# Kernel tuning notes

Measured on AMD Instinct MI355X. Metric: run time of the kernel, lower is better.

Reference implementation:

```python
import jax, jax.numpy as jnp
import numpy as np

N_NODES = 50000
N_GRAPHS = 128
IN_DIM = 512
HID = 512
N_LAYERS = 3


def setup_inputs() -> dict:
    key = jax.random.key(0)
    ks = jax.random.split(key, 12)
    inp = {
        "x": jax.random.normal(ks[0], (N_NODES, IN_DIM), dtype=jnp.float32),
        "walk2": jax.random.randint(ks[1], (3, N_NODES), 0, N_NODES, dtype=jnp.int32),
        "walk3": jax.random.randint(ks[2], (4, N_NODES), 0, N_NODES, dtype=jnp.int32),
        "walk4": jax.random.randint(ks[3], (5, N_NODES), 0, N_NODES, dtype=jnp.int32),
        "batch": jnp.sort(jax.random.randint(ks[4], (N_NODES,), 0, N_GRAPHS, dtype=jnp.int32)),
    }
    dims = [IN_DIM, HID, HID]
    for i in range(N_LAYERS):
        scale = 1.0 / np.sqrt(dims[i])
        inp[f"W{i}"] = jax.random.normal(ks[5 + i], (dims[i], HID), dtype=jnp.float32) * scale
        inp[f"b{i}"] = jnp.zeros((HID,), dtype=jnp.float32)
    return inp


def _gather_sum(z, walk):
    # walk: [L, N] node indices -> sum of gathered embeddings, [N, H]
    L, N = walk.shape
    return jnp.take(z, walk.reshape(-1), axis=0).reshape(L, N, z.shape[1]).sum(0)


def reference(x, walk2, walk3, walk4, batch, W0, b0, W1, b1, W2, b2):
    layers = [(W0, b0), (W1, b1), (W2, b2)]
    path_batch = jnp.take(batch, walk2[0])  # [N]
    counts = jax.ops.segment_sum(jnp.ones((path_batch.shape[0],), jnp.float32),
                                 path_batch, num_segments=N_GRAPHS)
    denom = jnp.maximum(counts, 1.0)[:, None]  # avoid div-by-zero for empty graphs
    z = x
    g = []
    for W, b in layers:
        z = z @ W + b  # [N, H]
        path_emb = _gather_sum(z, walk2) + _gather_sum(z, walk3) + _gather_sum(z, walk4)
        pooled = jax.ops.segment_sum(path_emb, path_batch, num_segments=N_GRAPHS) / denom
        g.append(pooled)
    return jnp.concatenate(g, axis=1)  # [N_GRAPHS, 3*H]
```

## Files before the change

kernel.cpp:

```cpp
#include <hip/hip_runtime.h>

#define N_NODES 50000
#define N_GRAPHS 128
#define HID 512

#define KSPAN  512
#define KSPLIT 98
#define KPAD   (KSPAN * KSPLIT)
#define NPANEL (KPAD / 16)

#define C8_OFF     0
#define C8_BYTES   ((size_t)N_GRAPHS * KPAD)
#define PSUM_OFF   (C8_OFF + C8_BYTES)
#define PSUM_BYTES ((size_t)N_GRAPHS * HID * 4)
#define COUNTS_OFF (PSUM_OFF + PSUM_BYTES)
#define ZERO_BYTES (COUNTS_OFF + 512)
#define APACK_OFF  ZERO_BYTES
#define APACK_BYTES ((size_t)NPANEL * 4 * 64 * 16)
#define PART_OFF   (APACK_OFF + APACK_BYTES)
#define PART_BYTES ((size_t)KSPLIT * N_GRAPHS * HID * 4)

typedef __attribute__((ext_vector_type(8))) short bf16x8;
typedef __attribute__((ext_vector_type(16))) float f32x16;
typedef const __attribute__((address_space(1))) void* gas_t;
typedef __attribute__((address_space(3))) void* las_t;

__global__ __launch_bounds__(256)
void build_c_kernel(const int* __restrict__ w2, const int* __restrict__ w3,
                    const int* __restrict__ w4, const int* __restrict__ batch,
                    unsigned int* __restrict__ C32, int* __restrict__ counts) {
    __shared__ int hist[N_GRAPHS];
    const int t = threadIdx.x;
    if (t < N_GRAPHS) hist[t] = 0;
    __syncthreads();
    const int i = blockIdx.x * 256 + t;
    if (i < N_NODES) {
        const int a = w2[i];
        const int g = batch[a];
        atomicAdd(&hist[g], 1);
        unsigned int* row = C32 + (size_t)g * (KPAD / 4);
        int nn[12];
        nn[0]  = a;
        nn[1]  = w2[N_NODES + i];
        nn[2]  = w2[2 * N_NODES + i];
        nn[3]  = w3[i];
        nn[4]  = w3[N_NODES + i];
        nn[5]  = w3[2 * N_NODES + i];
        nn[6]  = w3[3 * N_NODES + i];
        nn[7]  = w4[i];
        nn[8]  = w4[N_NODES + i];
        nn[9]  = w4[2 * N_NODES + i];
        nn[10] = w4[3 * N_NODES + i];
        nn[11] = w4[4 * N_NODES + i];
#pragma unroll
        for (int j = 0; j < 12; ++j) {
            const int nd = nn[j];
            atomicAdd(&row[nd >> 2], 1u << ((nd & 3) * 8));
        }
    }
    __syncthreads();
    if (t < N_GRAPHS) { const int hv = hist[t]; if (hv) atomicAdd(&counts[t], hv); }
}

__device__ inline unsigned pack_bf16(unsigned a, unsigned b) {
    return (__builtin_bit_cast(unsigned, (float)a) >> 16) |
           (__builtin_bit_cast(unsigned, (float)b) & 0xFFFF0000u);
}

__global__ __launch_bounds__(256)
void c8_to_apack_kernel(const unsigned char* __restrict__ C8,
                        uint4* __restrict__ Apack) {
    const int kp = blockIdx.x;
    const int t = threadIdx.x;
    const int mt = t >> 6;
    const int l = t & 63;
    const int row = mt * 32 + (l & 31);
    const int k0 = kp * 16 + 8 * (l >> 5);
    const uint2 b = *(const uint2*)(C8 + (size_t)row * KPAD + k0);
    uint4 o;
    o.x = pack_bf16(b.x & 0xFFu, (b.x >> 8) & 0xFFu);
    o.y = pack_bf16((b.x >> 16) & 0xFFu, b.x >> 24);
    o.z = pack_bf16(b.y & 0xFFu, (b.y >> 8) & 0xFFu);
    o.w = pack_bf16((b.y >> 16) & 0xFFu, b.y >> 24);
    Apack[(size_t)(kp * 4 + mt) * 64 + l] = o;
}

template <int ATOMIC>
__global__ __launch_bounds__(512, 4)
void pool_gemm4_kernel(const float* __restrict__ x,
                       const uint4* __restrict__ Apack,
                       float* __restrict__ dst) {
    __shared__ float lbuf[128 * 128];
    const int t = threadIdx.x;
    const int lane = t & 63;
    const int w = t >> 6;
    const int n = lane & 31;
    const int h = lane >> 5;
    const int nt = w & 3;
    const int mh = w >> 2;
    const int colbase = blockIdx.x * 128;
    const int ks = blockIdx.y;
    const int kbase = ks * KSPAN;

    f32x16 acc0, acc1;
#pragma unroll
    for (int r = 0; r < 16; ++r) { acc0[r] = 0.f; acc1[r] = 0.f; }

    for (int ch = 0; ch < 4; ++ch) {
        const int k0 = kbase + ch * 128;
        if (k0 >= N_NODES) break;
        if (k0 + 128 <= N_NODES) {
#pragma unroll
            for (int i = 0; i < 8; ++i) {
                const int rbase = w * 16 + 2 * i;
                const float* gp = x + (size_t)(k0 + rbase + (lane >> 5)) * HID
                                    + colbase + (lane & 31) * 4;
                las_t lp = (las_t)&lbuf[rbase * 128];
                __builtin_amdgcn_global_load_lds((gas_t)gp, lp, 16, 0, 0);
            }
        } else {
#pragma unroll
            for (int j = 0; j < 32; ++j) {
                const int idx = t + j * 512;
                const int r = idx >> 7, c = idx & 127;
                const int kg = k0 + r;
                lbuf[idx] = (kg < N_NODES) ? x[(size_t)kg * HID + colbase + c] : 0.f;
            }
        }
        __syncthreads();

        const int kp0 = k0 >> 4;
#pragma unroll
        for (int s = 0; s < 8; ++s) {
            unsigned bw[4];
#pragma unroll
            for (int j2 = 0; j2 < 4; ++j2) {
                const int kl = s * 16 + 8 * h + 2 * j2;
                const unsigned u0 = __builtin_bit_cast(unsigned, lbuf[kl * 128 + nt * 32 + n]);
                const unsigned u1 = __builtin_bit_cast(unsigned, lbuf[(kl + 1) * 128 + nt * 32 + n]);
                bw[j2] = (u0 >> 16) | (u1 & 0xFFFF0000u);
            }
            const uint4 bu = make_uint4(bw[0], bw[1], bw[2], bw[3]);
            const bf16x8 bf = __builtin_bit_cast(bf16x8, bu);
            const bf16x8 a0 = __builtin_bit_cast(bf16x8,
                Apack[(size_t)((kp0 + s) * 4 + 2 * mh) * 64 + lane]);
            const bf16x8 a1 = __builtin_bit_cast(bf16x8,
                Apack[(size_t)((kp0 + s) * 4 + 2 * mh + 1) * 64 + lane]);
            acc0 = __builtin_amdgcn_mfma_f32_32x32x16_bf16(a0, bf, acc0, 0, 0, 0);
            acc1 = __builtin_amdgcn_mfma_f32_32x32x16_bf16(a1, bf, acc1, 0, 0, 0);
        }
        __syncthreads();
    }

    float* outp = ATOMIC ? dst : dst + (size_t)ks * (N_GRAPHS * HID);
    const int col = colbase + nt * 32 + n;
#pragma unroll
    for (int r = 0; r < 16; ++r) {
        const int row0 = mh * 64 + (r & 3) + 8 * (r >> 2) + 4 * h;
        if (ATOMIC) {
            atomicAdd(&outp[(size_t)row0 * HID + col], acc0[r]);
            atomicAdd(&outp[(size_t)(row0 + 32) * HID + col], acc1[r]);
        } else {
            outp[(size_t)row0 * HID + col] = acc0[r];
            outp[(size_t)(row0 + 32) * HID + col] = acc1[r];
        }
    }
}

__global__ __launch_bounds__(256)
void reduce_part_kernel(const float* __restrict__ part, float* __restrict__ Psum) {
    const int id = blockIdx.x * 256 + threadIdx.x;
    float s0 = 0.f, s1 = 0.f;
    for (int k = 0; k + 2 <= KSPLIT; k += 2) {
        s0 += part[(size_t)k * (N_GRAPHS * HID) + id];
        s1 += part[(size_t)(k + 1) * (N_GRAPHS * HID) + id];
    }
    Psum[id] = s0 + s1;
}

__global__ __launch_bounds__(256)
void layer_gemm_kernel(const float* __restrict__ A, int lda, int scaleA,
                       const float* __restrict__ W,
                       const float* __restrict__ bias,
                       const int* __restrict__ counts,
                       float* __restrict__ out) {
    __shared__ float Alds[16][128];
    const int ct = blockIdx.x, rt = blockIdx.y, ksb = blockIdx.z;
    const int t = threadIdx.x;
    const int cc = ct * 64 + (t & 63);
    const int wv = t >> 6;
    const int k0 = ksb * 128;

    for (int idx = t; idx < 16 * 32; idx += 256) {
        const int rr = idx >> 5;
        const int kk = (idx & 31) * 4;
        const int row = rt * 16 + rr;
        float4 v = *(const float4*)&A[(size_t)row * lda + k0 + kk];
        if (scaleA) {
            const float inv = 1.f / (float)max(counts[row], 1);
            v.x *= inv; v.y *= inv; v.z *= inv; v.w *= inv;
        }
        *(float4*)&Alds[rr][kk] = v;
    }
    __syncthreads();

    const int r0 = rt * 16 + wv * 4;
    float a0 = 0.f, a1 = 0.f, a2 = 0.f, a3 = 0.f;
#pragma unroll 8
    for (int k = 0; k < 128; ++k) {
        const float wval = W[(size_t)(k0 + k) * HID + cc];
        a0 += Alds[wv * 4 + 0][k] * wval;
        a1 += Alds[wv * 4 + 1][k] * wval;
        a2 += Alds[wv * 4 + 2][k] * wval;
        a3 += Alds[wv * 4 + 3][k] * wval;
    }
    if (ksb == 0) {
        const float bc = bias[cc];
        a0 += (counts[r0 + 0] > 0 ? 12.f : 0.f) * bc;
        a1 += (counts[r0 + 1] > 0 ? 12.f : 0.f) * bc;
        a2 += (counts[r0 + 2] > 0 ? 12.f : 0.f) * bc;
        a3 += (counts[r0 + 3] > 0 ? 12.f : 0.f) * bc;
    }
    atomicAdd(&out[(size_t)(r0 + 0) * 1536 + cc], a0);
    atomicAdd(&out[(size_t)(r0 + 1) * 1536 + cc], a1);
    atomicAdd(&out[(size_t)(r0 + 2) * 1536 + cc], a2);
    atomicAdd(&out[(size_t)(r0 + 3) * 1536 + cc], a3);
}

extern "C" void kernel_launch(void* const* d_in, const int* in_sizes, int n_in,
                              void* d_out, int out_size, void* d_ws, size_t ws_size,
                              hipStream_t stream) {
    const float* x     = (const float*)d_in[0];
    const int*   w2    = (const int*)d_in[1];
    const int*   w3    = (const int*)d_in[2];
    const int*   w4    = (const int*)d_in[3];
    const int*   batch = (const int*)d_in[4];
    const float* W0    = (const float*)d_in[5];
    const float* b0    = (const float*)d_in[6];
    const float* W1    = (const float*)d_in[7];
    const float* b1    = (const float*)d_in[8];
    const float* W2    = (const float*)d_in[9];
    const float* b2    = (const float*)d_in[10];
    float* out = (float*)d_out;

    unsigned char* ws  = (unsigned char*)d_ws;
    unsigned int* C32  = (unsigned int*)(ws + C8_OFF);
    float* Psum        = (float*)(ws + PSUM_OFF);
    int* counts        = (int*)(ws + COUNTS_OFF);
    uint4* Apack       = (uint4*)(ws + APACK_OFF);
    float* part        = (float*)(ws + PART_OFF);
    const bool use_part = ws_size >= PART_OFF + PART_BYTES;

    hipMemsetAsync(d_ws, 0, ZERO_BYTES, stream);
    hipMemsetAsync(d_out, 0, (size_t)out_size * 4, stream);

    build_c_kernel<<<(N_NODES + 255) / 256, 256, 0, stream>>>(w2, w3, w4, batch, C32, counts);
    c8_to_apack_kernel<<<NPANEL, 256, 0, stream>>>((const unsigned char*)C32, Apack);

    if (use_part) {
        pool_gemm4_kernel<0><<<dim3(4, KSPLIT), 512, 0, stream>>>(x, Apack, part);
        reduce_part_kernel<<<256, 256, 0, stream>>>(part, Psum);
    } else {
        pool_gemm4_kernel<1><<<dim3(4, KSPLIT), 512, 0, stream>>>(x, Apack, Psum);
    }

    layer_gemm_kernel<<<dim3(8, 8, 4), 256, 0, stream>>>(Psum, HID, 1, W0, b0, counts, out);
    layer_gemm_kernel<<<dim3(8, 8, 4), 256, 0, stream>>>(out, 1536, 0, W1, b1, counts, out + 512);
    layer_gemm_kernel<<<dim3(8, 8, 4), 256, 0, stream>>>(out + 512, 1536, 0, W2, b2, counts, out + 1024);
}
```

Measured before the change: 276.4 us.

## Replace LDS-staged pooling GEMM with register-pipelined per-wave K-split and LDS reduction

The pooling GEMM (C x X) no longer stages X tiles through LDS with global_load_lds. Each wave now loads its B operand straight from global memory into registers, using a 3-deep software pipeline over 18 K-steps, and packs to bf16 with a perm instruction. Each wave owns its own K-slice of a 64x64 output region. The four waves in a block are summed through LDS before writing, which cuts the number of partial buffers from 98 to 44 and so reduces the later reduce pass. The risk is uncoalesced strided scalar loads from x and higher register pressure.

After: 266.8 us. -3.5%, faster.

```diff
diff --git a/kernel.cpp b/kernel.cpp
--- a/kernel.cpp
+++ b/kernel.cpp
@@ -4,10 +4,12 @@
 #define N_GRAPHS 128
 #define HID 512
 
-#define KSPAN  512
-#define KSPLIT 98
-#define KPAD   (KSPAN * KSPLIT)
-#define NPANEL (KPAD / 16)
+#define KSPAN   288
+#define NSTEP   18
+#define KS2     44
+#define KSPLIT  (KS2 * 4)
+#define KPAD    (KSPAN * KSPLIT)
+#define NPANEL  (KPAD / 16)
 
 #define C8_OFF     0
 #define C8_BYTES   ((size_t)N_GRAPHS * KPAD)
@@ -18,12 +20,10 @@
 #define APACK_OFF  ZERO_BYTES
 #define APACK_BYTES ((size_t)NPANEL * 4 * 64 * 16)
 #define PART_OFF   (APACK_OFF + APACK_BYTES)
-#define PART_BYTES ((size_t)KSPLIT * N_GRAPHS * HID * 4)
+#define PART_BYTES ((size_t)KS2 * N_GRAPHS * HID * 4)
 
 typedef __attribute__((ext_vector_type(8))) short bf16x8;
 typedef __attribute__((ext_vector_type(16))) float f32x16;
-typedef const __attribute__((address_space(1))) void* gas_t;
-typedef __attribute__((address_space(3))) void* las_t;
 
 __global__ __launch_bounds__(256)
 void build_c_kernel(const int* __restrict__ w2, const int* __restrict__ w3,
@@ -85,84 +85,128 @@
     Apack[(size_t)(kp * 4 + mt) * 64 + l] = o;
 }
 
+template <int GUARD>
+__device__ inline void issue_b(const float* __restrict__ xp, int krow,
+                               unsigned (&u)[16]) {
+#pragma unroll
+    for (int j = 0; j < 8; ++j) {
+        int k = krow + j;
+        if (GUARD) k = min(k, N_NODES - 1);
+        const float* p = xp + (size_t)k * HID;
+        u[j]     = __builtin_bit_cast(unsigned, p[0]);
+        u[8 + j] = __builtin_bit_cast(unsigned, p[32]);
+    }
+}
+
+__device__ inline f32x16 mfma_bf16(bf16x8 a, bf16x8 b, f32x16 c) {
+    return __builtin_amdgcn_mfma_f32_32x32x16_bf16(a, b, c, 0, 0, 0);
+}
+
+__device__ inline unsigned bpack(unsigned u0, unsigned u1) {
+    return __builtin_amdgcn_perm(u1, u0, 0x07060302u);
+}
+
+__device__ inline void step_mfma(const unsigned (&u)[16], const uint4 (&a)[2],
+                                 f32x16 (&acc)[2][2]) {
+    unsigned d0[4], d1[4];
+#pragma unroll
+    for (int jj = 0; jj < 4; ++jj) {
+        d0[jj] = bpack(u[2 * jj], u[2 * jj + 1]);
+        d1[jj] = bpack(u[8 + 2 * jj], u[8 + 2 * jj + 1]);
+    }
+    const bf16x8 b0 = __builtin_bit_cast(bf16x8, make_uint4(d0[0], d0[1], d0[2], d0[3]));
+    const bf16x8 b1 = __builtin_bit_cast(bf16x8, make_uint4(d1[0], d1[1], d1[2], d1[3]));
+    const bf16x8 a0 = __builtin_bit_cast(bf16x8, a[0]);
+    const bf16x8 a1 = __builtin_bit_cast(bf16x8, a[1]);
+    acc[0][0] = mfma_bf16(a0, b0, acc[0][0]);
+    acc[0][1] = mfma_bf16(a0, b1, acc[0][1]);
+    acc[1][0] = mfma_bf16(a1, b0, acc[1][0]);
+    acc[1][1] = mfma_bf16(a1, b1, acc[1][1]);
+}
+
+template <int GUARD>
+__device__ inline void run_k(const float* __restrict__ xp,
+                             const uint4* __restrict__ Apack,
+                             int kbase, int h, int lane, int rm,
+                             f32x16 (&acc)[2][2]) {
+    unsigned bu[3][16];
+    uint4 au[3][2];
+    const int kp0 = kbase >> 4;
+#pragma unroll
+    for (int s = 0; s < 3; ++s) {
+        issue_b<GUARD>(xp, kbase + s * 16 + 8 * h, bu[s]);
+        au[s][0] = Apack[(size_t)((kp0 + s) * 4 + rm * 2) * 64 + lane];
+        au[s][1] = Apack[(size_t)((kp0 + s) * 4 + rm * 2 + 1) * 64 + lane];
+    }
+#pragma unroll
+    for (int s = 0; s < NSTEP; ++s) {
+        const int slot = s % 3;
+        step_mfma(bu[slot], au[slot], acc);
+        if (s + 3 < NSTEP) {
+            issue_b<GUARD>(xp, kbase + (s + 3) * 16 + 8 * h, bu[slot]);
+            au[slot][0] = Apack[(size_t)((kp0 + s + 3) * 4 + rm * 2) * 64 + lane];
+            au[slot][1] = Apack[(size_t)((kp0 + s + 3) * 4 + rm * 2 + 1) * 64 + lane];
+        }
+    }
+}
+
 template <int ATOMIC>
-__global__ __launch_bounds__(512, 4)
-void pool_gemm4_kernel(const float* __restrict__ x,
+__global__ __launch_bounds__(256, 3)
+void pool_gemm5_kernel(const float* __restrict__ x,
                        const uint4* __restrict__ Apack,
                        float* __restrict__ dst) {
-    __shared__ float lbuf[128 * 128];
+    __shared__ float red[3][2][64 * 16];
     const int t = threadIdx.x;
     const int lane = t & 63;
     const int w = t >> 6;
     const int n = lane & 31;
     const int h = lane >> 5;
-    const int nt = w & 3;
-    const int mh = w >> 2;
-    const int colbase = blockIdx.x * 128;
-    const int ks = blockIdx.y;
+    const int region = blockIdx.x;
+    const int rm = region & 1;
+    const int rn = region >> 1;
+    const int ks = blockIdx.y * 4 + w;
     const int kbase = ks * KSPAN;
 
-    f32x16 acc0, acc1;
-#pragma unroll
-    for (int r = 0; r < 16; ++r) { acc0[r] = 0.f; acc1[r] = 0.f; }
-
-    for (int ch = 0; ch < 4; ++ch) {
-        const int k0 = kbase + ch * 128;
-        if (k0 >= N_NODES) break;
-        if (k0 + 128 <= N_NODES) {
-#pragma unroll
-            for (int i = 0; i < 8; ++i) {
-                const int rbase = w * 16 + 2 * i;
-                const float* gp = x + (size_t)(k0 + rbase + (lane >> 5)) * HID
-                                    + colbase + (lane & 31) * 4;
-                las_t lp = (las_t)&lbuf[rbase * 128];
-                __builtin_amdgcn_global_load_lds((gas_t)gp, lp, 16, 0, 0);
-            }
-        } else {
-#pragma unroll
-            for (int j = 0; j < 32; ++j) {
-                const int idx = t + j * 512;
-                const int r = idx >> 7, c = idx & 127;
-                const int kg = k0 + r;
-                lbuf[idx] = (kg < N_NODES) ? x[(size_t)kg * HID + colbase + c] : 0.f;
-            }
-        }
+    f32x16 acc[2][2];
+#pragma unroll
+    for (int p = 0; p < 2; ++p)
+#pragma unroll
+        for (int q = 0; q < 2; ++q)
+#pragma unroll
+            for (int r = 0; r < 16; ++r) acc[p][q][r] = 0.f;
+
+    const float* xp = x + rn * 64 + n;
+
+    if (kbase + KSPAN <= N_NODES) {
+        run_k<0>(xp, Apack, kbase, h, lane, rm, acc);
+    } else if (kbase < N_NODES) {
+        run_k<1>(xp, Apack, kbase, h, lane, rm, acc);
+    }
+
+    float* outp = ATOMIC ? dst : dst + (size_t)blockIdx.y * (N_GRAPHS * HID);
+#pragma unroll
+    for (int p = 0; p < 2; ++p) {
         __syncthreads();
-
-        const int kp0 = k0 >> 4;
-#pragma unroll
-        for (int s = 0; s < 8; ++s) {
-            unsigned bw[4];
-#pragma unroll
-            for (int j2 = 0; j2 < 4; ++j2) {
-                const int kl = s * 16 + 8 * h + 2 * j2;
-                const unsigned u0 = __builtin_bit_cast(unsigned, lbuf[kl * 128 + nt * 32 + n]);
-                const unsigned u1 = __builtin_bit_cast(unsigned, lbuf[(kl + 1) * 128 + nt * 32 + n]);
-                bw[j2] = (u0 >> 16) | (u1 & 0xFFFF0000u);
-            }
-            const uint4 bu = make_uint4(bw[0], bw[1], bw[2], bw[3]);
-            const bf16x8 bf = __builtin_bit_cast(bf16x8, bu);
-            const bf16x8 a0 = __builtin_bit_cast(bf16x8,
-                Apack[(size_t)((kp0 + s) * 4 + 2 * mh) * 64 + lane]);
-            const bf16x8 a1 = __builtin_bit_cast(bf16x8,
-                Apack[(size_t)((kp0 + s) * 4 + 2 * mh + 1) * 64 + lane]);
-            acc0 = __builtin_amdgcn_mfma_f32_32x32x16_bf16(a0, bf, acc0, 0, 0, 0);
-            acc1 = __builtin_amdgcn_mfma_f32_32x32x16_bf16(a1, bf, acc1, 0, 0, 0);
+        if (w > 0) {
+#pragma unroll
+            for (int q = 0; q < 2; ++q)
+#pragma unroll
+                for (int i = 0; i < 16; ++i)
+                    red[w - 1][q][i * 64 + lane] = acc[p][q][i];
         }
         __syncthreads();
-    }
-
-    float* outp = ATOMIC ? dst : dst + (size_t)ks * (N_GRAPHS * HID);
-    const int col = colbase + nt * 32 + n;
-#pragma unroll
-    for (int r = 0; r < 16; ++r) {
-        const int row0 = mh * 64 + (r & 3) + 8 * (r >> 2) + 4 * h;
-        if (ATOMIC) {
-            atomicAdd(&outp[(size_t)row0 * HID + col], acc0[r]);
-            atomicAdd(&outp[(size_t)(row0 + 32) * HID + col], acc1[r]);
-        } else {
-            outp[(size_t)row0 * HID + col] = acc0[r];
-            outp[(size_t)(row0 + 32) * HID + col] = acc1[r];
+        if (w == 0) {
+#pragma unroll
+            for (int q = 0; q < 2; ++q)
+#pragma unroll
+                for (int i = 0; i < 16; ++i) {
+                    const float v = acc[p][q][i] + red[0][q][i * 64 + lane] +
+                                    red[1][q][i * 64 + lane] + red[2][q][i * 64 + lane];
+                    const int row = rm * 64 + p * 32 + (i & 3) + 8 * (i >> 2) + 4 * h;
+                    const int col = rn * 64 + q * 32 + n;
+                    if (ATOMIC) atomicAdd(&outp[(size_t)row * HID + col], v);
+                    else        outp[(size_t)row * HID + col] = v;
+                }
         }
     }
 }
@@ -171,7 +215,7 @@
 void reduce_part_kernel(const float* __restrict__ part, float* __restrict__ Psum) {
     const int id = blockIdx.x * 256 + threadIdx.x;
     float s0 = 0.f, s1 = 0.f;
-    for (int k = 0; k + 2 <= KSPLIT; k += 2) {
+    for (int k = 0; k + 2 <= KS2; k += 2) {
         s0 += part[(size_t)k * (N_GRAPHS * HID) + id];
         s1 += part[(size_t)(k + 1) * (N_GRAPHS * HID) + id];
     }
@@ -258,10 +302,10 @@
     c8_to_apack_kernel<<<NPANEL, 256, 0, stream>>>((const unsigned char*)C32, Apack);
 
     if (use_part) {
-        pool_gemm4_kernel<0><<<dim3(4, KSPLIT), 512, 0, stream>>>(x, Apack, part);
+        pool_gemm5_kernel<0><<<dim3(16, KS2), 256, 0, stream>>>(x, Apack, part);
         reduce_part_kernel<<<256, 256, 0, stream>>>(part, Psum);
     } else {
-        pool_gemm4_kernel<1><<<dim3(4, KSPLIT), 512, 0, stream>>>(x, Apack, Psum);
+        pool_gemm5_kernel<1><<<dim3(16, KS2), 256, 0, stream>>>(x, Apack, Psum);
     }
 
     layer_gemm_kernel<<<dim3(8, 8, 4), 256, 0, stream>>>(Psum, HID, 1, W0, b0, counts, out);
```

## Restructure pooling GEMM to per-wave column slabs with full-M tiles and finer K split

Applied to the files above, without the earlier changes.

Replaces the pooling GEMM so that each block covers all 512 columns and all 128 graph rows for a 208-node K span, launching 241 blocks instead of a 4x98 grid. Each wave owns a private 64-column LDS slab, which removes block-wide __syncthreads. It loads the A panels for all four M tiles into registers and issues 8 MFMAs per K step, so each packed B fragment is reused across four A tiles. bf16 packing now uses v_perm. The trade-off is a much larger partial buffer (241 slices) for the reduce kernel to read, and higher register pressure (launch bounds 2 blocks per CU).

After: 291.0 us. +5.3%, slower.

```diff
diff --git a/kernel.cpp b/kernel.cpp
--- a/kernel.cpp
+++ b/kernel.cpp
@@ -4,10 +4,10 @@
 #define N_GRAPHS 128
 #define HID 512
 
-#define KSPAN  512
-#define KSPLIT 98
-#define KPAD   (KSPAN * KSPLIT)
-#define NPANEL (KPAD / 16)
+#define KSPAN   208
+#define KSPLIT  241
+#define KPAD    (KSPAN * KSPLIT)
+#define NPANEL  (KPAD / 16)
 
 #define C8_OFF     0
 #define C8_BYTES   ((size_t)N_GRAPHS * KPAD)
@@ -85,96 +85,128 @@
     Apack[(size_t)(kp * 4 + mt) * 64 + l] = o;
 }
 
+__device__ inline unsigned bpack(unsigned u0, unsigned u1) {
+    return __builtin_amdgcn_perm(u1, u0, 0x07060302u);
+}
+
+__device__ inline f32x16 mfma_bf16(bf16x8 a, bf16x8 b, f32x16 c) {
+    return __builtin_amdgcn_mfma_f32_32x32x16_bf16(a, b, c, 0, 0, 0);
+}
+
+template <int ROWS>
+__device__ inline void do_chunk(const float* __restrict__ x,
+                                const uint4* __restrict__ Apack,
+                                float* __restrict__ lb,
+                                int w, int lane, int s0, int kp0,
+                                f32x16 (&acc)[4][2]) {
+    const int cg = w * 64 + (lane & 15) * 4;
+    const int rsub = lane >> 4;
+
+    if (s0 + ROWS <= N_NODES) {
+#pragma unroll
+        for (int i = 0; i < ROWS / 4; ++i) {
+            const float* gp = x + (size_t)(s0 + 4 * i + rsub) * HID + cg;
+            las_t lp = (las_t)(lb + 4 * i * 64);
+            __builtin_amdgcn_global_load_lds((gas_t)gp, lp, 16, 0, 0);
+        }
+    } else {
+#pragma unroll
+        for (int i = 0; i < ROWS / 4; ++i) {
+            const int row = min(s0 + 4 * i + rsub, N_NODES - 1);
+            const float4 v = *(const float4*)(x + (size_t)row * HID + cg);
+            *(float4*)(lb + (4 * i + rsub) * 64 + (lane & 15) * 4) = v;
+        }
+    }
+
+    uint4 a[ROWS / 16][4];
+#pragma unroll
+    for (int s2 = 0; s2 < ROWS / 16; ++s2)
+#pragma unroll
+        for (int mt = 0; mt < 4; ++mt)
+            a[s2][mt] = Apack[(size_t)((kp0 + s2) * 4 + mt) * 64 + lane];
+
+    __builtin_amdgcn_s_waitcnt(0);
+
+    const int n = lane & 31;
+    const int h = lane >> 5;
+#pragma unroll
+    for (int s2 = 0; s2 < ROWS / 16; ++s2) {
+        unsigned b0w[4], b1w[4];
+#pragma unroll
+        for (int jj = 0; jj < 4; ++jj) {
+            const int r0 = s2 * 16 + 8 * h + 2 * jj;
+            const unsigned u00 = __builtin_bit_cast(unsigned, lb[r0 * 64 + n]);
+            const unsigned u01 = __builtin_bit_cast(unsigned, lb[(r0 + 1) * 64 + n]);
+            const unsigned u10 = __builtin_bit_cast(unsigned, lb[r0 * 64 + 32 + n]);
+            const unsigned u11 = __builtin_bit_cast(unsigned, lb[(r0 + 1) * 64 + 32 + n]);
+            b0w[jj] = bpack(u00, u01);
+            b1w[jj] = bpack(u10, u11);
+        }
+        const bf16x8 B0 = __builtin_bit_cast(bf16x8, make_uint4(b0w[0], b0w[1], b0w[2], b0w[3]));
+        const bf16x8 B1 = __builtin_bit_cast(bf16x8, make_uint4(b1w[0], b1w[1], b1w[2], b1w[3]));
+#pragma unroll
+        for (int mt = 0; mt < 4; ++mt) {
+            const bf16x8 af = __builtin_bit_cast(bf16x8, a[s2][mt]);
+            acc[mt][0] = mfma_bf16(af, B0, acc[mt][0]);
+            acc[mt][1] = mfma_bf16(af, B1, acc[mt][1]);
+        }
+    }
+}
+
 template <int ATOMIC>
-__global__ __launch_bounds__(512, 4)
-void pool_gemm4_kernel(const float* __restrict__ x,
+__global__ __launch_bounds__(512, 2)
+void pool_gemm6_kernel(const float* __restrict__ x,
                        const uint4* __restrict__ Apack,
                        float* __restrict__ dst) {
-    __shared__ float lbuf[128 * 128];
+    __shared__ float lbuf[8][32 * 64];
     const int t = threadIdx.x;
     const int lane = t & 63;
     const int w = t >> 6;
+    float* lb = &lbuf[w][0];
+
+    const int kbase = blockIdx.x * KSPAN;
+    const int kp_base = blockIdx.x * 13;
+
+    f32x16 acc[4][2];
+#pragma unroll
+    for (int mt = 0; mt < 4; ++mt)
+#pragma unroll
+        for (int q = 0; q < 2; ++q)
+#pragma unroll
+            for (int r = 0; r < 16; ++r) acc[mt][q][r] = 0.f;
+
+#pragma unroll
+    for (int ch = 0; ch < 6; ++ch)
+        do_chunk<32>(x, Apack, lb, w, lane, kbase + ch * 32, kp_base + ch * 2, acc);
+    do_chunk<16>(x, Apack, lb, w, lane, kbase + 192, kp_base + 12, acc);
+
     const int n = lane & 31;
     const int h = lane >> 5;
-    const int nt = w & 3;
-    const int mh = w >> 2;
-    const int colbase = blockIdx.x * 128;
-    const int ks = blockIdx.y;
-    const int kbase = ks * KSPAN;
-
-    f32x16 acc0, acc1;
-#pragma unroll
-    for (int r = 0; r < 16; ++r) { acc0[r] = 0.f; acc1[r] = 0.f; }
-
-    for (int ch = 0; ch < 4; ++ch) {
-        const int k0 = kbase + ch * 128;
-        if (k0 >= N_NODES) break;
-        if (k0 + 128 <= N_NODES) {
-#pragma unroll
-            for (int i = 0; i < 8; ++i) {
-                const int rbase = w * 16 + 2 * i;
-                const float* gp = x + (size_t)(k0 + rbase + (lane >> 5)) * HID
-                                    + colbase + (lane & 31) * 4;
-                las_t lp = (las_t)&lbuf[rbase * 128];
-                __builtin_amdgcn_global_load_lds((gas_t)gp, lp, 16, 0, 0);
+    float* outp = ATOMIC ? dst : dst + (size_t)blockIdx.x * (N_GRAPHS * HID);
+#pragma unroll
+    for (int mt = 0; mt < 4; ++mt)
+#pragma unroll
+        for (int q = 0; q < 2; ++q) {
+            const int col = w * 64 + q * 32 + n;
+#pragma unroll
+            for (int i = 0; i < 16; ++i) {
+                const int row = mt * 32 + (i & 3) + 8 * (i >> 2) + 4 * h;
+                if (ATOMIC) atomicAdd(&outp[(size_t)row * HID + col], acc[mt][q][i]);
+                else        outp[(size_t)row * HID + col] = acc[mt][q][i];
             }
-        } else {
-#pragma unroll
-            for (int j = 0; j < 32; ++j) {
-                const int idx = t + j * 512;
-                const int r = idx >> 7, c = idx & 127;
-                const int kg = k0 + r;
-                lbuf[idx] = (kg < N_NODES) ? x[(size_t)kg * HID + colbase + c] : 0.f;
-            }
-        }
-        __syncthreads();
-
-        const int kp0 = k0 >> 4;
-#pragma unroll
-        for (int s = 0; s < 8; ++s) {
-            unsigned bw[4];
-#pragma unroll
-            for (int j2 = 0; j2 < 4; ++j2) {
-                const int kl = s * 16 + 8 * h + 2 * j2;
-                const unsigned u0 = __builtin_bit_cast(unsigned, lbuf[kl * 128 + nt * 32 + n]);
-                const unsigned u1 = __builtin_bit_cast(unsigned, lbuf[(kl + 1) * 128 + nt * 32 + n]);
-                bw[j2] = (u0 >> 16) | (u1 & 0xFFFF0000u);
-            }
-            const uint4 bu = make_uint4(bw[0], bw[1], bw[2], bw[3]);
-            const bf16x8 bf = __builtin_bit_cast(bf16x8, bu);
-            const bf16x8 a0 = __builtin_bit_cast(bf16x8,
-                Apack[(size_t)((kp0 + s) * 4 + 2 * mh) * 64 + lane]);
-            const bf16x8 a1 = __builtin_bit_cast(bf16x8,
-                Apack[(size_t)((kp0 + s) * 4 + 2 * mh + 1) * 64 + lane]);
-            acc0 = __builtin_amdgcn_mfma_f32_32x32x16_bf16(a0, bf, acc0, 0, 0, 0);
-            acc1 = __builtin_amdgcn_mfma_f32_32x32x16_bf16(a1, bf, acc1, 0, 0, 0);
-        }
-        __syncthreads();
-    }
-
-    float* outp = ATOMIC ? dst : dst + (size_t)ks * (N_GRAPHS * HID);
-    const int col = colbase + nt * 32 + n;
-#pragma unroll
-    for (int r = 0; r < 16; ++r) {
-        const int row0 = mh * 64 + (r & 3) + 8 * (r >> 2) + 4 * h;
-        if (ATOMIC) {
-            atomicAdd(&outp[(size_t)row0 * HID + col], acc0[r]);
-            atomicAdd(&outp[(size_t)(row0 + 32) * HID + col], acc1[r]);
-        } else {
-            outp[(size_t)row0 * HID + col] = acc0[r];
-            outp[(size_t)(row0 + 32) * HID + col] = acc1[r];
-        }
-    }
+        }
 }
 
 __global__ __launch_bounds__(256)
 void reduce_part_kernel(const float* __restrict__ part, float* __restrict__ Psum) {
     const int id = blockIdx.x * 256 + threadIdx.x;
     float s0 = 0.f, s1 = 0.f;
-    for (int k = 0; k + 2 <= KSPLIT; k += 2) {
+    int k = 0;
+    for (; k + 2 <= KSPLIT; k += 2) {
         s0 += part[(size_t)k * (N_GRAPHS * HID) + id];
         s1 += part[(size_t)(k + 1) * (N_GRAPHS * HID) + id];
     }
+    for (; k < KSPLIT; ++k) s0 += part[(size_t)k * (N_GRAPHS * HID) + id];
     Psum[id] = s0 + s1;
 }
 
@@ -258,10 +290,10 @@
     c8_to_apack_kernel<<<NPANEL, 256, 0, stream>>>((const unsigned char*)C32, Apack);
 
     if (use_part) {
-        pool_gemm4_kernel<0><<<dim3(4, KSPLIT), 512, 0, stream>>>(x, Apack, part);
+        pool_gemm6_kernel<0><<<KSPLIT, 512, 0, stream>>>(x, Apack, part);
         reduce_part_kernel<<<256, 256, 0, stream>>>(part, Psum);
     } else {
-        pool_gemm4_kernel<1><<<dim3(4, KSPLIT), 512, 0, stream>>>(x, Apack, Psum);
+        pool_gemm6_kernel<1><<<KSPLIT, 512, 0, stream>>>(x, Apack, Psum);
     }
 
     layer_gemm_kernel<<<dim3(8, 8, 4), 256, 0, stream>>>(Psum, HID, 1, W0, b0, counts, out);
```

## Restructure pooled GEMM: stage A in LDS, stream x directly into registers

Applied to the files above, without the earlier changes.

Rewrites the pooling GEMM so each block copies its slice of the packed count matrix into LDS once. Each wave then reads x columns straight from global memory into registers with a two-stage software prefetch and packs them to bf16 with a byte-permute, and each wave computes all 128 graph rows. The K span is halved and the split count doubled, and the grid now uses two column halves instead of four. This drops the LDS staging of x and its barriers, but it issues strided per-row scalar global loads and doubles the partial buffer that the reduction must sum.

Result: slower. 287.8 us (+4.1%).

```diff
diff --git a/kernel.cpp b/kernel.cpp
--- a/kernel.cpp
+++ b/kernel.cpp
@@ -4,10 +4,10 @@
 #define N_GRAPHS 128
 #define HID 512
 
-#define KSPAN  512
-#define KSPLIT 98
-#define KPAD   (KSPAN * KSPLIT)
-#define NPANEL (KPAD / 16)
+#define KSPAN   256
+#define KSPLIT  196
+#define KPAD    (KSPAN * KSPLIT)
+#define NPANEL  (KPAD / 16)
 
 #define C8_OFF     0
 #define C8_BYTES   ((size_t)N_GRAPHS * KPAD)
@@ -22,8 +22,6 @@
 
 typedef __attribute__((ext_vector_type(8))) short bf16x8;
 typedef __attribute__((ext_vector_type(16))) float f32x16;
-typedef const __attribute__((address_space(1))) void* gas_t;
-typedef __attribute__((address_space(3))) void* las_t;
 
 __global__ __launch_bounds__(256)
 void build_c_kernel(const int* __restrict__ w2, const int* __restrict__ w3,
@@ -85,86 +83,98 @@
     Apack[(size_t)(kp * 4 + mt) * 64 + l] = o;
 }
 
+__device__ inline unsigned bpack(unsigned u0, unsigned u1) {
+    return __builtin_amdgcn_perm(u1, u0, 0x07060302u);
+}
+
+__device__ inline f32x16 mfma_bf16(bf16x8 a, bf16x8 b, f32x16 c) {
+    return __builtin_amdgcn_mfma_f32_32x32x16_bf16(a, b, c, 0, 0, 0);
+}
+
+template <int GUARD>
+__device__ inline void issue_b7(const float* __restrict__ xp, int krow,
+                                unsigned (&u)[8]) {
+#pragma unroll
+    for (int j = 0; j < 8; ++j) {
+        int k = krow + j;
+        if (GUARD) k = min(k, N_NODES - 1);
+        u[j] = __builtin_bit_cast(unsigned, xp[(size_t)k * HID]);
+    }
+}
+
+template <int GUARD>
+__device__ inline void run_k7(const float* __restrict__ xp,
+                              const uint4* __restrict__ ldsA,
+                              int kbase, int h, int lane,
+                              f32x16 (&acc)[4]) {
+    unsigned bu[2][8];
+    issue_b7<GUARD>(xp, kbase + 8 * h, bu[0]);
+    issue_b7<GUARD>(xp, kbase + 16 + 8 * h, bu[1]);
+#pragma unroll
+    for (int s = 0; s < KSPAN / 16; ++s) {
+        const int slot = s & 1;
+        uint4 a[4];
+#pragma unroll
+        for (int mt = 0; mt < 4; ++mt)
+            a[mt] = ldsA[(s * 4 + mt) * 64 + lane];
+        unsigned d[4];
+#pragma unroll
+        for (int jj = 0; jj < 4; ++jj)
+            d[jj] = bpack(bu[slot][2 * jj], bu[slot][2 * jj + 1]);
+        const bf16x8 B = __builtin_bit_cast(bf16x8, make_uint4(d[0], d[1], d[2], d[3]));
+        if (s + 2 < KSPAN / 16)
+            issue_b7<GUARD>(xp, kbase + (s + 2) * 16 + 8 * h, bu[slot]);
+#pragma unroll
+        for (int mt = 0; mt < 4; ++mt)
+            acc[mt] = mfma_bf16(__builtin_bit_cast(bf16x8, a[mt]), B, acc[mt]);
+    }
+}
+
 template <int ATOMIC>
 __global__ __launch_bounds__(512, 4)
-void pool_gemm4_kernel(const float* __restrict__ x,
+void pool_gemm7_kernel(const float* __restrict__ x,
                        const uint4* __restrict__ Apack,
                        float* __restrict__ dst) {
-    __shared__ float lbuf[128 * 128];
+    __shared__ uint4 ldsA[(KSPAN / 16) * 4 * 64];
     const int t = threadIdx.x;
     const int lane = t & 63;
     const int w = t >> 6;
     const int n = lane & 31;
     const int h = lane >> 5;
-    const int nt = w & 3;
-    const int mh = w >> 2;
-    const int colbase = blockIdx.x * 128;
+    const int chalf = blockIdx.x;
     const int ks = blockIdx.y;
     const int kbase = ks * KSPAN;
-
-    f32x16 acc0, acc1;
-#pragma unroll
-    for (int r = 0; r < 16; ++r) { acc0[r] = 0.f; acc1[r] = 0.f; }
-
-    for (int ch = 0; ch < 4; ++ch) {
-        const int k0 = kbase + ch * 128;
-        if (k0 >= N_NODES) break;
-        if (k0 + 128 <= N_NODES) {
-#pragma unroll
-            for (int i = 0; i < 8; ++i) {
-                const int rbase = w * 16 + 2 * i;
-                const float* gp = x + (size_t)(k0 + rbase + (lane >> 5)) * HID
-                                    + colbase + (lane & 31) * 4;
-                las_t lp = (las_t)&lbuf[rbase * 128];
-                __builtin_amdgcn_global_load_lds((gas_t)gp, lp, 16, 0, 0);
-            }
-        } else {
-#pragma unroll
-            for (int j = 0; j < 32; ++j) {
-                const int idx = t + j * 512;
-                const int r = idx >> 7, c = idx & 127;
-                const int kg = k0 + r;
-                lbuf[idx] = (kg < N_NODES) ? x[(size_t)kg * HID + colbase + c] : 0.f;
-            }
+    const int kp0 = ks * (KSPAN / 16);
+
+    {
+        const uint4* src = Apack + (size_t)kp0 * 4 * 64;
+#pragma unroll
+        for (int i = 0; i < 8; ++i)
+            ldsA[t + i * 512] = src[t + i * 512];
+    }
+    __syncthreads();
+
+    f32x16 acc[4];
+#pragma unroll
+    for (int mt = 0; mt < 4; ++mt)
+#pragma unroll
+        for (int r = 0; r < 16; ++r) acc[mt][r] = 0.f;
+
+    const int col = chalf * 256 + w * 32 + n;
+    const float* xp = x + col;
+
+    if (kbase + KSPAN <= N_NODES) run_k7<0>(xp, ldsA, kbase, h, lane, acc);
+    else                          run_k7<1>(xp, ldsA, kbase, h, lane, acc);
+
+    float* outp = ATOMIC ? dst : dst + (size_t)ks * (N_GRAPHS * HID);
+#pragma unroll
+    for (int mt = 0; mt < 4; ++mt)
+#pragma unroll
+        for (int i = 0; i < 16; ++i) {
+            const int row = mt * 32 + (i & 3) + 8 * (i >> 2) + 4 * h;
+            if (ATOMIC) atomicAdd(&outp[(size_t)row * HID + col], acc[mt][i]);
+            else        outp[(size_t)row * HID + col] = acc[mt][i];
         }
-        __syncthreads();
-
-        const int kp0 = k0 >> 4;
-#pragma unroll
-        for (int s = 0; s < 8; ++s) {
-            unsigned bw[4];
-#pragma unroll
-            for (int j2 = 0; j2 < 4; ++j2) {
-                const int kl = s * 16 + 8 * h + 2 * j2;
-                const unsigned u0 = __builtin_bit_cast(unsigned, lbuf[kl * 128 + nt * 32 + n]);
-                const unsigned u1 = __builtin_bit_cast(unsigned, lbuf[(kl + 1) * 128 + nt * 32 + n]);
-                bw[j2] = (u0 >> 16) | (u1 & 0xFFFF0000u);
-            }
-            const uint4 bu = make_uint4(bw[0], bw[1], bw[2], bw[3]);
-            const bf16x8 bf = __builtin_bit_cast(bf16x8, bu);
-            const bf16x8 a0 = __builtin_bit_cast(bf16x8,
-                Apack[(size_t)((kp0 + s) * 4 + 2 * mh) * 64 + lane]);
-            const bf16x8 a1 = __builtin_bit_cast(bf16x8,
-                Apack[(size_t)((kp0 + s) * 4 + 2 * mh + 1) * 64 + lane]);
-            acc0 = __builtin_amdgcn_mfma_f32_32x32x16_bf16(a0, bf, acc0, 0, 0, 0);
-            acc1 = __builtin_amdgcn_mfma_f32_32x32x16_bf16(a1, bf, acc1, 0, 0, 0);
-        }
-        __syncthreads();
-    }
-
-    float* outp = ATOMIC ? dst : dst + (size_t)ks * (N_GRAPHS * HID);
-    const int col = colbase + nt * 32 + n;
-#pragma unroll
-    for (int r = 0; r < 16; ++r) {
-        const int row0 = mh * 64 + (r & 3) + 8 * (r >> 2) + 4 * h;
-        if (ATOMIC) {
-            atomicAdd(&outp[(size_t)row0 * HID + col], acc0[r]);
-            atomicAdd(&outp[(size_t)(row0 + 32) * HID + col], acc1[r]);
-        } else {
-            outp[(size_t)row0 * HID + col] = acc0[r];
-            outp[(size_t)(row0 + 32) * HID + col] = acc1[r];
-        }
-    }
 }
 
 __global__ __launch_bounds__(256)
@@ -258,10 +268,10 @@
     c8_to_apack_kernel<<<NPANEL, 256, 0, stream>>>((const unsigned char*)C32, Apack);
 
     if (use_part) {
-        pool_gemm4_kernel<0><<<dim3(4, KSPLIT), 512, 0, stream>>>(x, Apack, part);
+        pool_gemm7_kernel<0><<<dim3(2, KSPLIT), 512, 0, stream>>>(x, Apack, part);
         reduce_part_kernel<<<256, 256, 0, stream>>>(part, Psum);
     } else {
-        pool_gemm4_kernel<1><<<dim3(4, KSPLIT), 512, 0, stream>>>(x, Apack, Psum);
+        pool_gemm7_kernel<1><<<dim3(2, KSPLIT), 512, 0, stream>>>(x, Apack, Psum);
     }
 
     layer_gemm_kernel<<<dim3(8, 8, 4), 256, 0, stream>>>(Psum, HID, 1, W0, b0, counts, out);
```
